# Optimization experiments

Hardware: AMD Instinct MI355X
Metric: run time of the kernel (lower is better)

The kernel has to match this reference:

```python
import jax, jax.numpy as jnp
import numpy as np

B, S = 8, 2048  # batch, seq_len; D == S required by matmul(value, qk)


def setup_inputs() -> dict:
    key = jax.random.key(0)
    kq, kk, kv = jax.random.split(key, 3)
    return {
        "query": jax.random.normal(kq, (B, S, S), dtype=jnp.float32),
        "key": jax.random.normal(kk, (B, S, S), dtype=jnp.float32),
        "value": jax.random.normal(kv, (B, S, S), dtype=jnp.float32),
        "attn_mask": jnp.zeros((S, S), dtype=jnp.float32),
    }


def reference(query, key, value, attn_mask):
    # qk = query @ key^T  -> [B, S, S]
    qk = jnp.einsum("bqd,bkd->bqk", query, key)
    # dropout with p=0.0 is the identity
    # softmax over the last dim (torch .softmax() intended dim=-1)
    qk = jax.nn.softmax(qk, axis=-1)
    # matmul(value, qk): [B, S, S] @ [B, S, S] -> [B, S, S]
    out = jnp.einsum("bsd,bdk->bsk", value, qk)
    return out
```

## Files before the change

kernel.cpp:

```cpp
#include <hip/hip_runtime.h>
#include <hip/hip_fp16.h>

typedef _Float16 f16;
typedef _Float16 f16x8 __attribute__((ext_vector_type(8)));
typedef _Float16 f16x4 __attribute__((ext_vector_type(4)));
typedef float f32x4 __attribute__((ext_vector_type(4)));

#define SEQ 2048
#define BATCH 8

__device__ __forceinline__ void gl2lds16(const f16* g, f16* l) {
  __builtin_amdgcn_global_load_lds((const __attribute__((address_space(1))) void*)g,
                                   (__attribute__((address_space(3))) void*)l,
                                   16, 0, 0);
}

__global__ __launch_bounds__(256) void cast_kernel(const float* __restrict__ in,
                                                   f16* __restrict__ out, int n4) {
  int i = blockIdx.x * 256 + threadIdx.x;
  if (i < n4) {
    float4 v = ((const float4*)in)[i];
    f16x4 h;
    h[0] = (f16)v.x; h[1] = (f16)v.y; h[2] = (f16)v.z; h[3] = (f16)v.w;
    ((f16x4*)out)[i] = h;
  }
}

__global__ __launch_bounds__(256) void gemm_nt(const f16* __restrict__ A,
                                               const f16* __restrict__ Bt,
                                               float* __restrict__ C,
                                               int K, int N,
                                               long long sA, long long sB, long long sC) {
  const f16* Ab = A + blockIdx.z * sA;
  const f16* Bb = Bt + blockIdx.z * sB;
  float* Cb = C + blockIdx.z * sC;
  const int m0 = blockIdx.y * 128, n0 = blockIdx.x * 128;

  __shared__ f16 As[128][32];
  __shared__ f16 Bs[128][32];

  const int tid = threadIdx.x;
  const int wave = tid >> 6, lane = tid & 63;
  const int wm = (wave >> 1) << 6;
  const int wn = (wave & 1) << 6;
  const int q = lane >> 4, ml = lane & 15;

  const int lrow = lane >> 2;
  const int lcol = (lane & 3) * 8;

  f32x4 acc[4][4];
#pragma unroll
  for (int i = 0; i < 4; i++)
#pragma unroll
    for (int j = 0; j < 4; j++) acc[i][j] = (f32x4){0.f, 0.f, 0.f, 0.f};

  for (int k0 = 0; k0 < K; k0 += 32) {
#pragma unroll
    for (int i = 0; i < 2; i++) {
      const int rb = (i * 4 + wave) * 16;
      gl2lds16(Ab + (size_t)(m0 + rb + lrow) * K + k0 + lcol, &As[rb][0]);
      gl2lds16(Bb + (size_t)(n0 + rb + lrow) * K + k0 + lcol, &Bs[rb][0]);
    }
    __syncthreads();

    f16x8 af[4], bf[4];
#pragma unroll
    for (int i = 0; i < 4; i++) af[i] = *(const f16x8*)&As[wm + i * 16 + ml][q * 8];
#pragma unroll
    for (int j = 0; j < 4; j++) bf[j] = *(const f16x8*)&Bs[wn + j * 16 + ml][q * 8];
#pragma unroll
    for (int i = 0; i < 4; i++)
#pragma unroll
      for (int j = 0; j < 4; j++)
        acc[i][j] = __builtin_amdgcn_mfma_f32_16x16x32_f16(af[i], bf[j], acc[i][j], 0, 0, 0);
    __syncthreads();
  }

#pragma unroll
  for (int i = 0; i < 4; i++) {
    const int row = m0 + wm + i * 16 + q * 4;
#pragma unroll
    for (int j = 0; j < 4; j++) {
      const int col = n0 + wn + j * 16 + ml;
      float* cp = Cb + (size_t)row * N + col;
      cp[0] = acc[i][j][0];
      cp[(size_t)N] = acc[i][j][1];
      cp[2 * (size_t)N] = acc[i][j][2];
      cp[3 * (size_t)N] = acc[i][j][3];
    }
  }
}

__global__ __launch_bounds__(256) void row_stats(const float* __restrict__ qk,
                                                 float* __restrict__ mrow,
                                                 float* __restrict__ zrow) {
  const size_t row = blockIdx.x;
  const float4* p = (const float4*)(qk + row * (size_t)SEQ);
  const int t = threadIdx.x;
  float4 a = p[t];
  float4 b = p[t + 256];
  float mx = fmaxf(fmaxf(fmaxf(a.x, a.y), fmaxf(a.z, a.w)),
                   fmaxf(fmaxf(b.x, b.y), fmaxf(b.z, b.w)));
  __shared__ float red[8];
#pragma unroll
  for (int o = 32; o > 0; o >>= 1) mx = fmaxf(mx, __shfl_xor(mx, o, 64));
  if ((t & 63) == 0) red[t >> 6] = mx;
  __syncthreads();
  mx = fmaxf(fmaxf(red[0], red[1]), fmaxf(red[2], red[3]));
  float s = __expf(a.x - mx) + __expf(a.y - mx) + __expf(a.z - mx) + __expf(a.w - mx) +
            __expf(b.x - mx) + __expf(b.y - mx) + __expf(b.z - mx) + __expf(b.w - mx);
#pragma unroll
  for (int o = 32; o > 0; o >>= 1) s += __shfl_xor(s, o, 64);
  if ((t & 63) == 0) red[4 + (t >> 6)] = s;
  __syncthreads();
  if (t == 0) {
    mrow[row] = mx;
    zrow[row] = red[4] + red[5] + red[6] + red[7];
  }
}

__global__ __launch_bounds__(256) void transpose_exp(const float* __restrict__ qk,
                                                     const float* __restrict__ mrow,
                                                     const float* __restrict__ zrow,
                                                     f16* __restrict__ PT) {
  const int b = blockIdx.z;
  const int d0 = blockIdx.y * 64, k0 = blockIdx.x * 64;
  const float* qb = qk + (size_t)b * SEQ * SEQ;
  f16* pb = PT + (size_t)b * SEQ * SEQ;
  __shared__ float T[64][65];
  const int t = threadIdx.x;
  const int rr = t >> 4, cc = (t & 15) * 4;
#pragma unroll
  for (int ch = 0; ch < 4; ch++) {
    const int r = rr + ch * 16;
    const int d = d0 + r;
    const float m = mrow[(size_t)b * SEQ + d];
    const float rz = 1.0f / zrow[(size_t)b * SEQ + d];
    float4 v = *(const float4*)(qb + (size_t)d * SEQ + k0 + cc);
    T[cc + 0][r] = __expf(v.x - m) * rz;
    T[cc + 1][r] = __expf(v.y - m) * rz;
    T[cc + 2][r] = __expf(v.z - m) * rz;
    T[cc + 3][r] = __expf(v.w - m) * rz;
  }
  __syncthreads();
  const int r2 = t >> 2, c2 = (t & 3) * 16;
  f16x8 o0, o1;
#pragma unroll
  for (int j = 0; j < 8; j++) o0[j] = (f16)T[r2][c2 + j];
#pragma unroll
  for (int j = 0; j < 8; j++) o1[j] = (f16)T[r2][c2 + 8 + j];
  f16* dst = pb + (size_t)(k0 + r2) * SEQ + d0 + c2;
  *(f16x8*)dst = o0;
  *(f16x8*)(dst + 8) = o1;
}

extern "C" void kernel_launch(void* const* d_in, const int* in_sizes, int n_in,
                              void* d_out, int out_size, void* d_ws, size_t ws_size,
                              hipStream_t stream) {
  const float* Q = (const float*)d_in[0];
  const float* Kf = (const float*)d_in[1];
  const float* V = (const float*)d_in[2];
  float* out = (float*)d_out;

  const size_t nElem = (size_t)BATCH * SEQ * SEQ;
  f16* Qh = (f16*)d_ws;
  f16* Kh = Qh + nElem;
  f16* Vh = Kh + nElem;
  f16* PT = Vh + nElem;
  float* qk = (float*)(PT + nElem);
  float* mrow = qk + nElem;
  float* zrow = mrow + (size_t)BATCH * SEQ;

  const int n4 = (int)(nElem / 4);
  dim3 cgrid(n4 / 256);
  cast_kernel<<<cgrid, 256, 0, stream>>>(Q, Qh, n4);
  cast_kernel<<<cgrid, 256, 0, stream>>>(Kf, Kh, n4);
  cast_kernel<<<cgrid, 256, 0, stream>>>(V, Vh, n4);

  const long long sb = (long long)SEQ * SEQ;
  dim3 ggrid(SEQ / 128, SEQ / 128, BATCH);
  gemm_nt<<<ggrid, 256, 0, stream>>>(Qh, Kh, qk, SEQ, SEQ, sb, sb, sb);

  row_stats<<<dim3(BATCH * SEQ), 256, 0, stream>>>(qk, mrow, zrow);

  transpose_exp<<<dim3(SEQ / 64, SEQ / 64, BATCH), 256, 0, stream>>>(qk, mrow, zrow, PT);

  gemm_nt<<<ggrid, 256, 0, stream>>>(Vh, PT, out, SEQ, SEQ, sb, sb, sb);
}
```

Before: 888.0 us.

## Compute K·Qᵀ directly to drop transpose, use column softmax stats and 32x32 MFMA

The first GEMM now swaps its operands to produce the transposed score matrix directly. Softmax statistics therefore become column-wise, computed with a chunked online max/sum pass plus a combine kernel. A simple elementwise scale kernel replaces the LDS transpose kernel. The GEMM inner loop switches from 16x16x32 to 32x32x16 MFMA tiles with a new accumulator layout and store pattern. The partial-stats buffers reuse the Qh workspace after the first GEMM; this is fine because Qh is not read again.

```diff
diff --git a/kernel.cpp b/kernel.cpp
--- a/kernel.cpp
+++ b/kernel.cpp
@@ -5,9 +5,11 @@
 typedef _Float16 f16x8 __attribute__((ext_vector_type(8)));
 typedef _Float16 f16x4 __attribute__((ext_vector_type(4)));
 typedef float f32x4 __attribute__((ext_vector_type(4)));
+typedef float f32x16 __attribute__((ext_vector_type(16)));
 
 #define SEQ 2048
 #define BATCH 8
+#define NCHUNK 16
 
 __device__ __forceinline__ void gl2lds16(const f16* g, f16* l) {
   __builtin_amdgcn_global_load_lds((const __attribute__((address_space(1))) void*)g,
@@ -43,16 +45,18 @@
   const int wave = tid >> 6, lane = tid & 63;
   const int wm = (wave >> 1) << 6;
   const int wn = (wave & 1) << 6;
-  const int q = lane >> 4, ml = lane & 15;
+  const int l31 = lane & 31, h = lane >> 5;
 
   const int lrow = lane >> 2;
   const int lcol = (lane & 3) * 8;
 
-  f32x4 acc[4][4];
+  f32x16 acc[2][2];
 #pragma unroll
-  for (int i = 0; i < 4; i++)
+  for (int i = 0; i < 2; i++)
 #pragma unroll
-    for (int j = 0; j < 4; j++) acc[i][j] = (f32x4){0.f, 0.f, 0.f, 0.f};
+    for (int j = 0; j < 2; j++)
+#pragma unroll
+      for (int r = 0; r < 16; r++) acc[i][j][r] = 0.f;
 
   for (int k0 = 0; k0 < K; k0 += 32) {
 #pragma unroll
@@ -63,95 +67,88 @@
     }
     __syncthreads();
 
-    f16x8 af[4], bf[4];
 #pragma unroll
-    for (int i = 0; i < 4; i++) af[i] = *(const f16x8*)&As[wm + i * 16 + ml][q * 8];
-#pragma unroll
-    for (int j = 0; j < 4; j++) bf[j] = *(const f16x8*)&Bs[wn + j * 16 + ml][q * 8];
-#pragma unroll
-    for (int i = 0; i < 4; i++)
-#pragma unroll
-      for (int j = 0; j < 4; j++)
-        acc[i][j] = __builtin_amdgcn_mfma_f32_16x16x32_f16(af[i], bf[j], acc[i][j], 0, 0, 0);
+    for (int s = 0; s < 2; s++) {
+      f16x8 a0 = *(const f16x8*)&As[wm + l31][s * 16 + h * 8];
+      f16x8 a1 = *(const f16x8*)&As[wm + 32 + l31][s * 16 + h * 8];
+      f16x8 b0 = *(const f16x8*)&Bs[wn + l31][s * 16 + h * 8];
+      f16x8 b1 = *(const f16x8*)&Bs[wn + 32 + l31][s * 16 + h * 8];
+      acc[0][0] = __builtin_amdgcn_mfma_f32_32x32x16_f16(a0, b0, acc[0][0], 0, 0, 0);
+      acc[0][1] = __builtin_amdgcn_mfma_f32_32x32x16_f16(a0, b1, acc[0][1], 0, 0, 0);
+      acc[1][0] = __builtin_amdgcn_mfma_f32_32x32x16_f16(a1, b0, acc[1][0], 0, 0, 0);
+      acc[1][1] = __builtin_amdgcn_mfma_f32_32x32x16_f16(a1, b1, acc[1][1], 0, 0, 0);
+    }
     __syncthreads();
   }
 
 #pragma unroll
-  for (int i = 0; i < 4; i++) {
-    const int row = m0 + wm + i * 16 + q * 4;
+  for (int i = 0; i < 2; i++) {
 #pragma unroll
-    for (int j = 0; j < 4; j++) {
-      const int col = n0 + wn + j * 16 + ml;
-      float* cp = Cb + (size_t)row * N + col;
-      cp[0] = acc[i][j][0];
-      cp[(size_t)N] = acc[i][j][1];
-      cp[2 * (size_t)N] = acc[i][j][2];
-      cp[3 * (size_t)N] = acc[i][j][3];
+    for (int j = 0; j < 2; j++) {
+      const int colb = n0 + wn + j * 32 + l31;
+      const int rowb = m0 + wm + i * 32 + 4 * h;
+#pragma unroll
+      for (int r = 0; r < 16; r++) {
+        const int row = rowb + (r & 3) + 8 * (r >> 2);
+        Cb[(size_t)row * N + colb] = acc[i][j][r];
+      }
     }
   }
 }
 
-__global__ __launch_bounds__(256) void row_stats(const float* __restrict__ qk,
-                                                 float* __restrict__ mrow,
-                                                 float* __restrict__ zrow) {
-  const size_t row = blockIdx.x;
-  const float4* p = (const float4*)(qk + row * (size_t)SEQ);
-  const int t = threadIdx.x;
-  float4 a = p[t];
-  float4 b = p[t + 256];
-  float mx = fmaxf(fmaxf(fmaxf(a.x, a.y), fmaxf(a.z, a.w)),
-                   fmaxf(fmaxf(b.x, b.y), fmaxf(b.z, b.w)));
-  __shared__ float red[8];
-#pragma unroll
-  for (int o = 32; o > 0; o >>= 1) mx = fmaxf(mx, __shfl_xor(mx, o, 64));
-  if ((t & 63) == 0) red[t >> 6] = mx;
-  __syncthreads();
-  mx = fmaxf(fmaxf(red[0], red[1]), fmaxf(red[2], red[3]));
-  float s = __expf(a.x - mx) + __expf(a.y - mx) + __expf(a.z - mx) + __expf(a.w - mx) +
-            __expf(b.x - mx) + __expf(b.y - mx) + __expf(b.z - mx) + __expf(b.w - mx);
-#pragma unroll
-  for (int o = 32; o > 0; o >>= 1) s += __shfl_xor(s, o, 64);
-  if ((t & 63) == 0) red[4 + (t >> 6)] = s;
-  __syncthreads();
-  if (t == 0) {
-    mrow[row] = mx;
-    zrow[row] = red[4] + red[5] + red[6] + red[7];
+__global__ __launch_bounds__(256) void colstats_part(const float* __restrict__ G,
+                                                     float* __restrict__ pm,
+                                                     float* __restrict__ ps) {
+  const int b = blockIdx.z, chunk = blockIdx.y;
+  const int q = blockIdx.x * 256 + threadIdx.x;
+  const int rows = SEQ / NCHUNK;
+  const float* p = G + (size_t)b * SEQ * SEQ + (size_t)chunk * rows * SEQ + q;
+  float m = -3.0e38f, s = 0.f;
+#pragma unroll 4
+  for (int k = 0; k < rows; k++) {
+    float x = p[(size_t)k * SEQ];
+    if (x > m) { s = s * __expf(m - x) + 1.f; m = x; }
+    else       { s += __expf(x - m); }
   }
+  const size_t o = ((size_t)chunk * BATCH + b) * SEQ + q;
+  pm[o] = m;
+  ps[o] = s;
 }
 
-__global__ __launch_bounds__(256) void transpose_exp(const float* __restrict__ qk,
-                                                     const float* __restrict__ mrow,
-                                                     const float* __restrict__ zrow,
-                                                     f16* __restrict__ PT) {
-  const int b = blockIdx.z;
-  const int d0 = blockIdx.y * 64, k0 = blockIdx.x * 64;
-  const float* qb = qk + (size_t)b * SEQ * SEQ;
-  f16* pb = PT + (size_t)b * SEQ * SEQ;
-  __shared__ float T[64][65];
-  const int t = threadIdx.x;
-  const int rr = t >> 4, cc = (t & 15) * 4;
+__global__ __launch_bounds__(256) void colstats_combine(const float* __restrict__ pm,
+                                                        const float* __restrict__ ps,
+                                                        float* __restrict__ mrow,
+                                                        float* __restrict__ rzrow) {
+  const int b = blockIdx.y;
+  const int q = blockIdx.x * 256 + threadIdx.x;
+  float m = -3.0e38f, s = 0.f;
 #pragma unroll
-  for (int ch = 0; ch < 4; ch++) {
-    const int r = rr + ch * 16;
-    const int d = d0 + r;
-    const float m = mrow[(size_t)b * SEQ + d];
-    const float rz = 1.0f / zrow[(size_t)b * SEQ + d];
-    float4 v = *(const float4*)(qb + (size_t)d * SEQ + k0 + cc);
-    T[cc + 0][r] = __expf(v.x - m) * rz;
-    T[cc + 1][r] = __expf(v.y - m) * rz;
-    T[cc + 2][r] = __expf(v.z - m) * rz;
-    T[cc + 3][r] = __expf(v.w - m) * rz;
+  for (int c = 0; c < NCHUNK; c++) {
+    const size_t o = ((size_t)c * BATCH + b) * SEQ + q;
+    float mc = pm[o], sc = ps[o];
+    if (mc > m) { s = s * __expf(m - mc) + sc; m = mc; }
+    else        { s += sc * __expf(mc - m); }
   }
-  __syncthreads();
-  const int r2 = t >> 2, c2 = (t & 3) * 16;
-  f16x8 o0, o1;
-#pragma unroll
-  for (int j = 0; j < 8; j++) o0[j] = (f16)T[r2][c2 + j];
-#pragma unroll
-  for (int j = 0; j < 8; j++) o1[j] = (f16)T[r2][c2 + 8 + j];
-  f16* dst = pb + (size_t)(k0 + r2) * SEQ + d0 + c2;
-  *(f16x8*)dst = o0;
-  *(f16x8*)(dst + 8) = o1;
+  mrow[(size_t)b * SEQ + q] = m;
+  rzrow[(size_t)b * SEQ + q] = 1.f / s;
+}
+
+__global__ __launch_bounds__(256) void scale_kernel(const float* __restrict__ G,
+                                                    const float* __restrict__ mrow,
+                                                    const float* __restrict__ rzrow,
+                                                    f16* __restrict__ PT) {
+  const int i = blockIdx.x * 256 + threadIdx.x;
+  const int b = i >> 20;
+  const int cg = i & (SEQ / 4 - 1);
+  float4 g = ((const float4*)G)[i];
+  float4 m4 = ((const float4*)(mrow + (size_t)b * SEQ))[cg];
+  float4 z4 = ((const float4*)(rzrow + (size_t)b * SEQ))[cg];
+  f16x4 o;
+  o[0] = (f16)(__expf(g.x - m4.x) * z4.x);
+  o[1] = (f16)(__expf(g.y - m4.y) * z4.y);
+  o[2] = (f16)(__expf(g.z - m4.z) * z4.z);
+  o[3] = (f16)(__expf(g.w - m4.w) * z4.w);
+  ((f16x4*)PT)[i] = o;
 }
 
 extern "C" void kernel_launch(void* const* d_in, const int* in_sizes, int n_in,
@@ -167,9 +164,11 @@
   f16* Kh = Qh + nElem;
   f16* Vh = Kh + nElem;
   f16* PT = Vh + nElem;
-  float* qk = (float*)(PT + nElem);
-  float* mrow = qk + nElem;
-  float* zrow = mrow + (size_t)BATCH * SEQ;
+  float* G = (float*)(PT + nElem);
+  float* mrow = G + nElem;
+  float* rzrow = mrow + (size_t)BATCH * SEQ;
+  float* pm = (float*)Qh;
+  float* ps = pm + (size_t)NCHUNK * BATCH * SEQ;
 
   const int n4 = (int)(nElem / 4);
   dim3 cgrid(n4 / 256);
@@ -179,11 +178,12 @@
 
   const long long sb = (long long)SEQ * SEQ;
   dim3 ggrid(SEQ / 128, SEQ / 128, BATCH);
-  gemm_nt<<<ggrid, 256, 0, stream>>>(Qh, Kh, qk, SEQ, SEQ, sb, sb, sb);
+  gemm_nt<<<ggrid, 256, 0, stream>>>(Kh, Qh, G, SEQ, SEQ, sb, sb, sb);
 
-  row_stats<<<dim3(BATCH * SEQ), 256, 0, stream>>>(qk, mrow, zrow);
+  colstats_part<<<dim3(SEQ / 256, NCHUNK, BATCH), 256, 0, stream>>>(G, pm, ps);
+  colstats_combine<<<dim3(SEQ / 256, BATCH), 256, 0, stream>>>(pm, ps, mrow, rzrow);
 
-  transpose_exp<<<dim3(SEQ / 64, SEQ / 64, BATCH), 256, 0, stream>>>(qk, mrow, zrow, PT);
+  scale_kernel<<<dim3(n4 / 256), 256, 0, stream>>>(G, mrow, rzrow, PT);
 
   gemm_nt<<<ggrid, 256, 0, stream>>>(Vh, PT, out, SEQ, SEQ, sb, sb, sb);
 }
```

After: 874.2 us. Within noise of the previous version (-1.6%).
